# Optimization experiments

Measured on AMD Instinct MI355X. Metric: run time of the kernel, lower is better.

## Reference

```python
import jax, jax.numpy as jnp
import numpy as np

N_NODES = 100000
N_EDGES = 640000
NIN = 128
NOUT = 128


def setup_inputs() -> dict:
    key = jax.random.key(0)
    ks = jax.random.split(key, 10)
    scale = 1.0 / np.sqrt(NIN)
    x = jax.random.normal(ks[0], (N_NODES, NIN), dtype=jnp.float32)
    edge_index = jax.random.randint(ks[1], (2, N_EDGES), 0, N_NODES, dtype=jnp.int64)
    edge_attr = jnp.zeros((N_EDGES, 1), dtype=jnp.float32)
    Wk = jax.random.uniform(ks[2], (NIN, NOUT), jnp.float32, -scale, scale)
    bk = jax.random.uniform(ks[3], (NOUT,), jnp.float32, -scale, scale)
    Wq = jax.random.uniform(ks[4], (NIN, NOUT), jnp.float32, -scale, scale)
    bq = jax.random.uniform(ks[5], (NOUT,), jnp.float32, -scale, scale)
    Wv = jax.random.uniform(ks[6], (NIN, NOUT), jnp.float32, -scale, scale)
    bv = jax.random.uniform(ks[7], (NOUT,), jnp.float32, -scale, scale)
    Wskip = jax.random.uniform(ks[8], (NIN, NOUT), jnp.float32, -scale, scale)
    bias = jax.random.uniform(ks[9], (NOUT,), jnp.float32, -scale, scale)
    return {
        "x": x, "edge_index": edge_index, "edge_attr": edge_attr,
        "Wk": Wk, "bk": bk, "Wq": Wq, "bq": bq,
        "Wv": Wv, "bv": bv, "Wskip": Wskip, "bias": bias,
    }


def reference(x, edge_index, edge_attr, Wk, bk, Wq, bq, Wv, bv, Wskip, bias):
    # PyG ResGatedGraphConv: out_i = W_skip x_i + b + sum_{j->i} sigmoid(k_i + q_j) * v_j
    # k = lin_key(x) (applied to dst), q = lin_query(x) (src), v = lin_value(x) (src)
    src, dst = edge_index[0], edge_index[1]
    k = x @ Wk + bk            # [N, NOUT]
    q = x @ Wq + bq            # [N, NOUT]
    v = x @ Wv + bv            # [N, NOUT]
    eta = jax.nn.sigmoid(k[dst] + q[src])   # [E, NOUT] per-edge gate
    msg = eta * v[src]                       # [E, NOUT]
    agg = jax.ops.segment_sum(msg, dst, num_segments=x.shape[0])  # [N, NOUT]
    return agg + x @ Wskip + bias
```

## Files before the change

kernel.cpp:

```cpp
#include <hip/hip_runtime.h>
#include <hip/hip_bf16.h>

typedef __bf16 v4bf __attribute__((ext_vector_type(4)));
typedef __bf16 v8bf __attribute__((ext_vector_type(8)));
typedef float  v16f __attribute__((ext_vector_type(16)));
typedef float  f4v  __attribute__((ext_vector_type(4)));
typedef unsigned int u4v __attribute__((ext_vector_type(4)));

#define LOG2E 1.44269504088896340736f

__device__ __forceinline__ unsigned short f2bf(float f) {
    union { float f; unsigned int u; } a; a.f = f;
    unsigned int r = a.u + 0x7FFFu + ((a.u >> 16) & 1u);
    return (unsigned short)(r >> 16);
}

__device__ __forceinline__ void unpack8v(u4v w, float* f) {
    #pragma unroll
    for (int i = 0; i < 4; ++i) {
        f[2 * i]     = __uint_as_float(w[i] << 16);
        f[2 * i + 1] = __uint_as_float(w[i] & 0xFFFF0000u);
    }
}

__global__ __launch_bounds__(256) void prep_count(
    const float* __restrict__ Wk, const float* __restrict__ Wq,
    const float* __restrict__ Wv, const float* __restrict__ Ws,
    unsigned short* __restrict__ Wt,
    const int* __restrict__ ei, int E,
    int* __restrict__ deg, int* __restrict__ pos)
{
    int i = blockIdx.x * 256 + threadIdx.x;
    if (i < 65536) {
        int m = i >> 14;
        int r = i & 16383;
        int n = r >> 7, k = r & 127;
        const float* W = (m == 0) ? Wk : (m == 1) ? Wq : (m == 2) ? Wv : Ws;
        float scale = (m == 0) ? -LOG2E : (m == 1) ? LOG2E : 1.0f;
        Wt[i] = f2bf(W[k * 128 + n] * scale);
    }
    for (int e = i; e < E; e += 131072) {
        pos[e] = atomicAdd(&deg[ei[E + e]], 1);
    }
}

__global__ __launch_bounds__(256) void scan_fused(
    const int* __restrict__ deg, int N, int* __restrict__ rowStart,
    int* __restrict__ flag)
{
    __shared__ int sums[256];
    __shared__ int red[256];
    const int t = threadIdx.x;
    const int b = blockIdx.x;
    const int base = b * 1024 + t * 4;
    int d0 = 0, d1 = 0, d2 = 0, d3 = 0;
    if (base + 3 < N) {
        int4 dd = *(const int4*)(deg + base);
        d0 = dd.x; d1 = dd.y; d2 = dd.z; d3 = dd.w;
    } else {
        if (base + 0 < N) d0 = deg[base + 0];
        if (base + 1 < N) d1 = deg[base + 1];
        if (base + 2 < N) d2 = deg[base + 2];
        if (base + 3 < N) d3 = deg[base + 3];
    }
    int tot = d0 + d1 + d2 + d3;
    sums[t] = tot;
    __syncthreads();
    #pragma unroll
    for (int off = 1; off < 256; off <<= 1) {
        int v = (t >= off) ? sums[t - off] : 0;
        __syncthreads();
        sums[t] += v;
        __syncthreads();
    }
    if (t == 255) {
        __threadfence();
        atomicExch(&flag[b], sums[255] + 1);
    }
    int partial = 0;
    for (int j = t; j < b; j += 256) {
        int v;
        do { v = atomicAdd(&flag[j], 0); } while (v == 0);
        partial += v - 1;
    }
    red[t] = partial;
    __syncthreads();
    #pragma unroll
    for (int off = 128; off > 0; off >>= 1) {
        if (t < off) red[t] += red[t + off];
        __syncthreads();
    }
    const int coff = red[0];
    int excl = sums[t] - tot + coff;
    if (base + 0 < N) rowStart[base + 0] = excl;
    if (base + 1 < N) rowStart[base + 1] = excl + d0;
    if (base + 2 < N) rowStart[base + 2] = excl + d0 + d1;
    if (base + 3 < N) rowStart[base + 3] = excl + d0 + d1 + d2;
}

__global__ __launch_bounds__(1024, 4) void gemm_fill(
    const float* __restrict__ x, int N,
    const unsigned short* __restrict__ Wt,
    const float* __restrict__ bk, const float* __restrict__ bq,
    const float* __restrict__ bv, const float* __restrict__ bs,
    unsigned short* __restrict__ kws, unsigned short* __restrict__ qv,
    float* __restrict__ out,
    const int* __restrict__ ei, int E,
    const int* __restrict__ rowStart, const int* __restrict__ pos,
    int* __restrict__ elist)
{
    for (int e = blockIdx.x * 1024 + threadIdx.x; e < E; e += gridDim.x * 1024) {
        elist[rowStart[ei[E + e]] + pos[e]] = ei[e];
    }

    __shared__ __align__(16) unsigned short xs[32 * 132];
    const int t   = threadIdx.x;
    const int wid = t >> 6;
    const int m   = wid >> 2;
    const int ct  = wid & 3;
    const int l   = t & 63;
    const int col = ct * 32 + (l & 31);
    const int kb  = (l >> 5) * 8;

    v8bf b[8];
    {
        const unsigned short* wp = Wt + m * 16384 + col * 128 + kb;
        #pragma unroll
        for (int c = 0; c < 8; ++c) b[c] = *(const v8bf*)(wp + c * 16);
    }
    const float* bvec = (m == 0) ? bk : (m == 1) ? bq : (m == 2) ? bv : bs;
    const float bcol = bvec[col] * ((m == 0) ? -LOG2E : (m == 1) ? LOG2E : 1.0f);
    unsigned short* dst; int dstride;
    if (m == 0)      { dst = kws;      dstride = 128; }
    else if (m == 1) { dst = qv;       dstride = 256; }
    else             { dst = qv + 128; dstride = 256; }

    const int srow = t >> 5;
    const int sk4  = (t & 31) << 2;
    const int rowb = 4 * (l >> 5);

    const int ntiles = (N + 31) >> 5;
    int tile = blockIdx.x;
    if (tile >= ntiles) return;

    float4 stg = make_float4(0.f, 0.f, 0.f, 0.f);
    {
        int gr = tile * 32 + srow;
        if (gr < N) stg = *(const float4*)(x + (size_t)gr * 128 + sk4);
    }

    const unsigned short* ap = xs + (l & 31) * 132 + kb;

    while (true) {
        ushort4 pk;
        pk.x = f2bf(stg.x); pk.y = f2bf(stg.y);
        pk.z = f2bf(stg.z); pk.w = f2bf(stg.w);
        *(ushort4*)(xs + srow * 132 + sk4) = pk;
        __syncthreads();

        int next = tile + gridDim.x;
        if (next < ntiles) {
            int gr = next * 32 + srow;
            stg = (gr < N) ? *(const float4*)(x + (size_t)gr * 128 + sk4)
                           : make_float4(0.f, 0.f, 0.f, 0.f);
        }

        v16f acc = {};
        #pragma unroll
        for (int c = 0; c < 8; ++c) {
            v4bf a0 = *(const v4bf*)(ap + c * 16);
            v4bf a1 = *(const v4bf*)(ap + c * 16 + 4);
            v8bf a = __builtin_shufflevector(a0, a1, 0, 1, 2, 3, 4, 5, 6, 7);
            acc = __builtin_amdgcn_mfma_f32_32x32x16_bf16(a, b[c], acc, 0, 0, 0);
        }

        const int r0 = tile * 32 + rowb;
        if (m == 3) {
            #pragma unroll
            for (int reg = 0; reg < 16; ++reg) {
                int row = r0 + (reg & 3) + 8 * (reg >> 2);
                if (row < N) out[(size_t)row * 128 + col] = acc[reg] + bcol;
            }
        } else {
            #pragma unroll
            for (int reg = 0; reg < 16; ++reg) {
                int row = r0 + (reg & 3) + 8 * (reg >> 2);
                if (row < N) dst[(size_t)row * dstride + col] = f2bf(acc[reg] + bcol);
            }
        }

        tile = next;
        if (tile >= ntiles) break;
        __syncthreads();
    }
}

__global__ __launch_bounds__(256, 4) void gather_agg(
    const int* __restrict__ rowStart, const int* __restrict__ deg,
    const int* __restrict__ elist,
    const unsigned short* __restrict__ kws,
    const unsigned short* __restrict__ qv,
    float* __restrict__ out, int N)
{
    int gid = blockIdx.x * 256 + threadIdx.x;
    int node = gid >> 4;
    if (node >= N) return;
    const int fo = (gid & 15) << 3;

    float* orow = out + (size_t)node * 128 + fo;
    f4v o0 = *(const f4v*)(orow);
    f4v o1 = *(const f4v*)(orow + 4);
    u4v kraw = *(const u4v*)(kws + (size_t)node * 128 + fo);
    const int p0 = rowStart[node];
    const int dg = deg[node];
    const int e  = p0 + dg;
    const int eL = e - 1;

    float nkf[8];
    unpack8v(kraw, nkf);
    float acc[8] = {};

    const unsigned short* qvb = qv + fo;

    for (int base = p0; base < e; base += 4) {
        int idx[4];
        #pragma unroll
        for (int s = 0; s < 4; ++s) {
            int pp = base + s;
            idx[s] = elist[pp < e ? pp : eL];
        }
        u4v qr[4], vr[4];
        #pragma unroll
        for (int s = 0; s < 4; ++s) {
            const unsigned short* r = qvb + (idx[s] << 8);
            qr[s] = *(const u4v*)(r);
            vr[s] = *(const u4v*)(r + 128);
        }
        #pragma unroll
        for (int s = 0; s < 4; ++s) {
            u4v vv = vr[s];
            if (base + s >= e) { vv[0] = 0u; vv[1] = 0u; vv[2] = 0u; vv[3] = 0u; }
            float qf[8], vf[8];
            unpack8v(qr[s], qf);
            unpack8v(vv, vf);
            #pragma unroll
            for (int j = 0; j < 8; ++j) {
                float ex = __builtin_amdgcn_exp2f(nkf[j] - qf[j]);
                acc[j] = fmaf(__builtin_amdgcn_rcpf(1.0f + ex), vf[j], acc[j]);
            }
        }
    }

    o0[0] += acc[0]; o0[1] += acc[1]; o0[2] += acc[2]; o0[3] += acc[3];
    o1[0] += acc[4]; o1[1] += acc[5]; o1[2] += acc[6]; o1[3] += acc[7];
    *(f4v*)(orow)     = o0;
    *(f4v*)(orow + 4) = o1;
}

extern "C" void kernel_launch(void* const* d_in, const int* in_sizes, int n_in,
                              void* d_out, int out_size, void* d_ws, size_t ws_size,
                              hipStream_t stream) {
    const float* x    = (const float*)d_in[0];
    const int*   ei   = (const int*)d_in[1];
    const float* Wk   = (const float*)d_in[3];
    const float* bk   = (const float*)d_in[4];
    const float* Wq   = (const float*)d_in[5];
    const float* bq   = (const float*)d_in[6];
    const float* Wv   = (const float*)d_in[7];
    const float* bv   = (const float*)d_in[8];
    const float* Ws   = (const float*)d_in[9];
    const float* bias = (const float*)d_in[10];

    const int N = in_sizes[0] / 128;
    const int E = in_sizes[1] / 2;
    float* out = (float*)d_out;

    unsigned short* kws = (unsigned short*)d_ws;
    unsigned short* qv  = kws + (size_t)N * 128;
    int* deg      = (int*)(qv + (size_t)N * 256);
    int* flag     = deg + N;
    int* rowStart = flag + 128;
    int* pos      = rowStart + N;
    int* elist    = pos + E;
    unsigned short* Wt = (unsigned short*)(elist + E);

    const int nChunks = (N + 1023) / 1024;

    hipMemsetAsync(deg, 0, (size_t)(N + 128) * sizeof(int), stream);

    prep_count<<<512, 256, 0, stream>>>(Wk, Wq, Wv, Ws, Wt, ei, E, deg, pos);
    scan_fused<<<nChunks, 256, 0, stream>>>(deg, N, rowStart, flag);
    gemm_fill<<<1024, 1024, 0, stream>>>(
        x, N, Wt, bk, bq, bv, bias, kws, qv, out, ei, E, rowStart, pos, elist);
    gather_agg<<<((size_t)N * 16 + 255) / 256, 256, 0, stream>>>(
        rowStart, deg, elist, kws, qv, out, N);
}
```

Measured before the change: 264.1 us.

## Fuse memset, degree count and scan into one cooperative kernel with grid syncs

Replaces the memset, the degree-count kernel and the decoupled-lookback scan kernel with a single cooperatively launched kernel. It zeroes the degree array, counts degrees, computes per-chunk scans and then chunk offsets, separated by grid-wide barriers. This removes two launches and the memset, and it drops the spin-waiting flag protocol. In exchange it adds three grid syncs and the overhead of a cooperative launch, and all 512 blocks must be co-resident on the device.

Result: slower. 525.7 us (+99.1%).

```diff
diff --git a/kernel.cpp b/kernel.cpp
--- a/kernel.cpp
+++ b/kernel.cpp
@@ -1,5 +1,8 @@
 #include <hip/hip_runtime.h>
 #include <hip/hip_bf16.h>
+#include <hip/hip_cooperative_groups.h>
+
+namespace cg = cooperative_groups;
 
 typedef __bf16 v4bf __attribute__((ext_vector_type(4)));
 typedef __bf16 v8bf __attribute__((ext_vector_type(8)));
@@ -23,14 +26,20 @@
     }
 }
 
-__global__ __launch_bounds__(256) void prep_count(
+__global__ __launch_bounds__(256) void prep_scan(
     const float* __restrict__ Wk, const float* __restrict__ Wq,
     const float* __restrict__ Wv, const float* __restrict__ Ws,
     unsigned short* __restrict__ Wt,
     const int* __restrict__ ei, int E,
-    int* __restrict__ deg, int* __restrict__ pos)
+    int* __restrict__ deg, int* __restrict__ pos, int N,
+    int* __restrict__ rowStart, int* __restrict__ chunkTot)
 {
-    int i = blockIdx.x * 256 + threadIdx.x;
+    cg::grid_group grid = cg::this_grid();
+    const int t = threadIdx.x;
+    const int b = blockIdx.x;
+    const int i = b * 256 + t;
+
+    if (i < N) deg[i] = 0;
     if (i < 65536) {
         int m = i >> 14;
         int r = i & 16383;
@@ -39,63 +48,61 @@
         float scale = (m == 0) ? -LOG2E : (m == 1) ? LOG2E : 1.0f;
         Wt[i] = f2bf(W[k * 128 + n] * scale);
     }
+    __threadfence();
+    grid.sync();
+
     for (int e = i; e < E; e += 131072) {
         pos[e] = atomicAdd(&deg[ei[E + e]], 1);
     }
-}
-
-__global__ __launch_bounds__(256) void scan_fused(
-    const int* __restrict__ deg, int N, int* __restrict__ rowStart,
-    int* __restrict__ flag)
-{
+    __threadfence();
+    grid.sync();
+
     __shared__ int sums[256];
     __shared__ int red[256];
-    const int t = threadIdx.x;
-    const int b = blockIdx.x;
+    const int nChunks = (N + 1023) >> 10;
     const int base = b * 1024 + t * 4;
     int d0 = 0, d1 = 0, d2 = 0, d3 = 0;
-    if (base + 3 < N) {
-        int4 dd = *(const int4*)(deg + base);
-        d0 = dd.x; d1 = dd.y; d2 = dd.z; d3 = dd.w;
-    } else {
-        if (base + 0 < N) d0 = deg[base + 0];
-        if (base + 1 < N) d1 = deg[base + 1];
-        if (base + 2 < N) d2 = deg[base + 2];
-        if (base + 3 < N) d3 = deg[base + 3];
-    }
-    int tot = d0 + d1 + d2 + d3;
-    sums[t] = tot;
-    __syncthreads();
-    #pragma unroll
-    for (int off = 1; off < 256; off <<= 1) {
-        int v = (t >= off) ? sums[t - off] : 0;
+    if (b < nChunks) {
+        if (base + 3 < N) {
+            int4 dd = *(const int4*)(deg + base);
+            d0 = dd.x; d1 = dd.y; d2 = dd.z; d3 = dd.w;
+        } else {
+            if (base + 0 < N) d0 = deg[base + 0];
+            if (base + 1 < N) d1 = deg[base + 1];
+            if (base + 2 < N) d2 = deg[base + 2];
+            if (base + 3 < N) d3 = deg[base + 3];
+        }
+        int tot = d0 + d1 + d2 + d3;
+        sums[t] = tot;
         __syncthreads();
-        sums[t] += v;
+        #pragma unroll
+        for (int off = 1; off < 256; off <<= 1) {
+            int v = (t >= off) ? sums[t - off] : 0;
+            __syncthreads();
+            sums[t] += v;
+            __syncthreads();
+        }
+        if (t == 255) chunkTot[b] = sums[255];
+    }
+    __threadfence();
+    grid.sync();
+
+    if (b < nChunks) {
+        red[t] = (t < b) ? chunkTot[t] : 0;
         __syncthreads();
-    }
-    if (t == 255) {
-        __threadfence();
-        atomicExch(&flag[b], sums[255] + 1);
-    }
-    int partial = 0;
-    for (int j = t; j < b; j += 256) {
-        int v;
-        do { v = atomicAdd(&flag[j], 0); } while (v == 0);
-        partial += v - 1;
-    }
-    red[t] = partial;
-    __syncthreads();
-    #pragma unroll
-    for (int off = 128; off > 0; off >>= 1) {
-        if (t < off) red[t] += red[t + off];
-        __syncthreads();
-    }
-    const int coff = red[0];
-    int excl = sums[t] - tot + coff;
-    if (base + 0 < N) rowStart[base + 0] = excl;
-    if (base + 1 < N) rowStart[base + 1] = excl + d0;
-    if (base + 2 < N) rowStart[base + 2] = excl + d0 + d1;
-    if (base + 3 < N) rowStart[base + 3] = excl + d0 + d1 + d2;
+        #pragma unroll
+        for (int off = 128; off > 0; off >>= 1) {
+            if (t < off) red[t] += red[t + off];
+            __syncthreads();
+        }
+        const int coff = red[0];
+        int tot = d0 + d1 + d2 + d3;
+        int excl = sums[t] - tot + coff;
+        if (base + 0 < N) rowStart[base + 0] = excl;
+        if (base + 1 < N) rowStart[base + 1] = excl + d0;
+        if (base + 2 < N) rowStart[base + 2] = excl + d0 + d1;
+        if (base + 3 < N) rowStart[base + 3] = excl + d0 + d1 + d2;
+    }
 }
 
 __global__ __launch_bounds__(1024, 4) void gemm_fill(
@@ -278,18 +285,26 @@
     unsigned short* kws = (unsigned short*)d_ws;
     unsigned short* qv  = kws + (size_t)N * 128;
     int* deg      = (int*)(qv + (size_t)N * 256);
-    int* flag     = deg + N;
-    int* rowStart = flag + 128;
+    int* chunkTot = deg + N;
+    int* rowStart = chunkTot + 128;
     int* pos      = rowStart + N;
     int* elist    = pos + E;
     unsigned short* Wt = (unsigned short*)(elist + E);
 
-    const int nChunks = (N + 1023) / 1024;
-
-    hipMemsetAsync(deg, 0, (size_t)(N + 128) * sizeof(int), stream);
-
-    prep_count<<<512, 256, 0, stream>>>(Wk, Wq, Wv, Ws, Wt, ei, E, deg, pos);
-    scan_fused<<<nChunks, 256, 0, stream>>>(deg, N, rowStart, flag);
+    {
+        unsigned short* Wt_ = Wt;
+        const int* ei_ = ei; int E_ = E; int N_ = N;
+        int* deg_ = deg; int* pos_ = pos; int* rowStart_ = rowStart;
+        int* chunkTot_ = chunkTot;
+        const float *Wk_ = Wk, *Wq_ = Wq, *Wv_ = Wv, *Ws_ = Ws;
+        void* args[] = { (void*)&Wk_, (void*)&Wq_, (void*)&Wv_, (void*)&Ws_,
+                         (void*)&Wt_, (void*)&ei_, (void*)&E_,
+                         (void*)&deg_, (void*)&pos_, (void*)&N_,
+                         (void*)&rowStart_, (void*)&chunkTot_ };
+        hipLaunchCooperativeKernel((void*)prep_scan, dim3(512), dim3(256),
+                                   args, 0, stream);
+    }
+
     gemm_fill<<<1024, 1024, 0, stream>>>(
         x, N, Wt, bk, bq, bv, bias, kws, qv, out, ei, E, rowStart, pos, elist);
     gather_agg<<<((size_t)N * 16 + 255) / 256, 256, 0, stream>>>(
```
